# Performance work log

Measured on AMD Instinct MI355X. Metric: run time of the kernel, lower is better.

## Reference

```python
import jax, jax.numpy as jnp
import numpy as np

SF = 2  # shrink_factor


def resize_bilinear_ac(x, oh, ow):
    """Bilinear resize with align_corners=True, NCHW, matches torch F.interpolate."""
    B, C, H, W = x.shape
    if (oh, ow) == (H, W):
        return x
    ys = jnp.linspace(0.0, H - 1, oh)
    y0 = jnp.floor(ys).astype(jnp.int32)
    y1 = jnp.clip(y0 + 1, 0, H - 1)
    wy = (ys - y0).astype(x.dtype)
    xs = jnp.linspace(0.0, W - 1, ow)
    x0 = jnp.floor(xs).astype(jnp.int32)
    x1 = jnp.clip(x0 + 1, 0, W - 1)
    wx = (xs - x0).astype(x.dtype)
    t = x[:, :, y0, :] * (1 - wy)[None, None, :, None] + x[:, :, y1, :] * wy[None, None, :, None]
    return t[:, :, :, x0] * (1 - wx) + t[:, :, :, x1] * wx


def conv1x1(x, W, b):
    # x: [B,C,H,W], W: [O,C], b: [O]
    return jnp.einsum('bchw,oc->bohw', x, W) + b[None, :, None, None]


def setup_inputs() -> dict:
    key = jax.random.key(0)
    ks = jax.random.split(key, 8)
    B, C, H, W = 4, 512, 129, 129
    Cqk = C // 8
    s = 1.0 / np.sqrt(C)
    return {
        'x': jax.random.normal(ks[0], (B, C, H, W), jnp.float32),
        'Wq': jax.random.normal(ks[1], (Cqk, C), jnp.float32) * s,
        'bq': jax.random.normal(ks[2], (Cqk,), jnp.float32) * s,
        'Wk': jax.random.normal(ks[3], (Cqk, C), jnp.float32) * s,
        'bk': jax.random.normal(ks[4], (Cqk,), jnp.float32) * s,
        'Wv': jax.random.normal(ks[5], (C, C), jnp.float32) * s,
        'bv': jax.random.normal(ks[6], (C,), jnp.float32) * s,
        'gamma': jax.random.normal(ks[7], (1,), jnp.float32) * 0.1,
    }


def reference(x, Wq, bq, Wk, bk, Wv, bv, gamma):
    B, C, H, W = x.shape
    h = (H - 1) // SF + 1
    w = (W - 1) // SF + 1
    xs = resize_bilinear_ac(x, h, w)  # [B,C,h,w]
    N = h * w
    q = conv1x1(xs, Wq, bq).reshape(B, -1, N)  # [B,Cqk,N]
    k = conv1x1(xs, Wk, bk).reshape(B, -1, N)  # [B,Cqk,N]
    v = conv1x1(xs, Wv, bv).reshape(B, -1, N)  # [B,C,N]
    # energy[b,n,m] = <q[:,n], k[:,m]>
    energy = jnp.einsum('bcn,bcm->bnm', q, k)  # [B,N,N]
    attention = jax.nn.softmax(energy, axis=-1)
    # out[b,c,n] = sum_m v[b,c,m] * attention[b,n,m]  (bmm(value, attention^T))
    out = jnp.einsum('bcm,bnm->bcn', v, attention).reshape(B, C, h, w)
    Hu = (h - 1) * SF + 1
    Wu = (w - 1) * SF + 1
    out = resize_bilinear_ac(out, Hu, Wu)
    out = gamma[0] * out + x
    return out, energy
```

## Files before the change

kernel.cpp:

```cpp
#include <hip/hip_runtime.h>
#include <hip/hip_bf16.h>
#include <cstdint>

#define BB 4
#define CC 512
#define CQK 64
#define HH 129
#define WW 129
#define HS 65
#define WSZ 65
#define NN 4225
#define NP 4352
#define KPV 4288
#define OUTSZ 34080768
#define ESZ 17850625

typedef unsigned short u16;
typedef __attribute__((ext_vector_type(8))) __bf16 bfrag;
typedef __attribute__((ext_vector_type(4))) float f4v;

__device__ inline u16 f2bf(float f) {
    union { float f; unsigned int u; } v; v.f = f;
    unsigned int u = v.u;
    return (u16)((u + 0x7FFFu + ((u >> 16) & 1u)) >> 16);
}

__device__ __forceinline__ void gload16(const u16* g, u16* l) {
    __builtin_amdgcn_global_load_lds(
        (const __attribute__((address_space(1))) void*)g,
        (__attribute__((address_space(3))) void*)l, 16, 0, 0);
}

__global__ __launch_bounds__(256) void cast_weights(const float* __restrict__ Wq,
                                                    const float* __restrict__ Wk,
                                                    const float* __restrict__ Wv,
                                                    u16* __restrict__ Wc) {
    int idx = blockIdx.x * 256 + threadIdx.x;
    if (idx >= 640 * 512) return;
    int o = idx >> 9, c = idx & 511;
    float v = (o < 64) ? Wq[o * 512 + c] : (o < 128) ? Wk[(o - 64) * 512 + c] : Wv[(o - 128) * 512 + c];
    Wc[idx] = f2bf(v);
}

__global__ __launch_bounds__(256) void subsample_t(const float* __restrict__ x, u16* __restrict__ XsT) {
    __shared__ u16 tile[64][65];
    int nt = blockIdx.x, ct = blockIdx.y, b = blockIdx.z;
    int t = threadIdx.x;
#pragma unroll
    for (int l = 0; l < 16; ++l) {
        int e = t + l * 256;
        int ci = e >> 6, nj = e & 63;
        int n = nt * 64 + nj;
        int nc = n < (NN - 1) ? n : (NN - 1);
        int i = nc / 65, j = nc % 65;
        int c = ct * 64 + ci;
        float v = x[(((size_t)b * CC + c) * HH + 2 * i) * WW + 2 * j];
        tile[ci][nj] = f2bf(v);
    }
    __syncthreads();
#pragma unroll
    for (int l = 0; l < 16; ++l) {
        int e = t + l * 256;
        int nj = e >> 6, ci = e & 63;
        XsT[((size_t)b * NP + nt * 64 + nj) * 512 + ct * 64 + ci] = tile[ci][nj];
    }
}

template <int MODE>
__global__ __launch_bounds__(256) void gemm_nt(const u16* __restrict__ Abase,
                                               const u16* __restrict__ Bbase,
                                               int K, int lda, int ldb,
                                               float* __restrict__ outF,
                                               u16* __restrict__ out1, u16* __restrict__ out2,
                                               const float* __restrict__ bq,
                                               const float* __restrict__ bk,
                                               const float* __restrict__ bv,
                                               float* __restrict__ psums) {
    __shared__ __align__(16) u16 As[128 * 64];
    __shared__ __align__(16) u16 Bs[128 * 64];

    const int z = blockIdx.z;
    const u16* A; const u16* Bm;
    if (MODE == 0) { A = Abase;                          Bm = Bbase + (size_t)z * NP * 512; }
    if (MODE == 1) { A = Abase + (size_t)z * NP * 128;   Bm = Bbase + (size_t)z * NP * 128 + 64; }

    const size_t m0 = (size_t)blockIdx.y * 128;
    const size_t n0 = (size_t)blockIdx.x * 128;
    const u16* Ab = A + m0 * lda;
    const u16* Bb = Bm + n0 * ldb;

    const int tid = threadIdx.x;
    const int lane = tid & 63, w = tid >> 6;
    const int wr = w >> 1, wc = w & 1;
    const int frow = lane & 15, fk = (lane >> 4) * 8;

    f4v acc[4][4];
#pragma unroll
    for (int i = 0; i < 4; ++i)
#pragma unroll
        for (int j = 0; j < 4; ++j) acc[i][j] = (f4v){0.f, 0.f, 0.f, 0.f};

    for (int kt = 0; kt < K; kt += 64) {
        if (kt) __syncthreads();
#pragma unroll
        for (int it = 0; it < 4; ++it) {
            int cb = (it * 4 + w) * 64;
            int chunk = cb + lane;
            int r = chunk >> 3;
            int kc = (chunk & 7) << 3;
            gload16(Ab + (size_t)r * lda + kt + kc, &As[cb * 8]);
            gload16(Bb + (size_t)r * ldb + kt + kc, &Bs[cb * 8]);
        }
        __syncthreads();
#pragma unroll
        for (int ks = 0; ks < 2; ++ks) {
            bfrag af[4], bf[4];
#pragma unroll
            for (int i = 0; i < 4; ++i)
                af[i] = *(const bfrag*)&As[(wr * 64 + i * 16 + frow) * 64 + ks * 32 + fk];
#pragma unroll
            for (int j = 0; j < 4; ++j)
                bf[j] = *(const bfrag*)&Bs[(wc * 64 + j * 16 + frow) * 64 + ks * 32 + fk];
#pragma unroll
            for (int i = 0; i < 4; ++i)
#pragma unroll
                for (int j = 0; j < 4; ++j)
                    acc[i][j] = __builtin_amdgcn_mfma_f32_16x16x32_bf16(af[i], bf[j], acc[i][j], 0, 0, 0);
        }
    }

    const int rbase = (lane >> 4) * 4, cbase = lane & 15;

    if (MODE == 0) {
        u16* out1b = out1 + (size_t)z * NP * 128;
        u16* out2b = out2 + (size_t)z * 512 * NP;
#pragma unroll
        for (int i = 0; i < 4; ++i)
#pragma unroll
            for (int j = 0; j < 4; ++j) {
                size_t row0 = m0 + wr * 64 + i * 16 + rbase;
                size_t col = n0 + wc * 64 + j * 16 + cbase;
#pragma unroll
                for (int r = 0; r < 4; ++r) {
                    int o = (int)(row0 + r);
                    float bias = (o < 64) ? bq[o] : (o < 128) ? bk[o - 64] : bv[o - 128];
                    u16 bb = f2bf(acc[i][j][r] + bias);
                    if (o < 128) out1b[col * 128 + o] = bb;
                    else out2b[(size_t)(o - 128) * NP + col] = bb;
                }
            }
    } else {
        float* eb = outF + (size_t)z * ESZ;
        u16* Pb = out1 + (size_t)z * NP * NP;
        float psl[4][4];
#pragma unroll
        for (int i = 0; i < 4; ++i)
#pragma unroll
            for (int r = 0; r < 4; ++r) psl[i][r] = 0.f;
#pragma unroll
        for (int i = 0; i < 4; ++i)
#pragma unroll
            for (int j = 0; j < 4; ++j) {
                size_t row0 = m0 + wr * 64 + i * 16 + rbase;
                size_t col = n0 + wc * 64 + j * 16 + cbase;
#pragma unroll
                for (int r = 0; r < 4; ++r) {
                    float v = acc[i][j][r];
                    size_t ro = row0 + r;
                    float pe = (col < NN) ? __expf(v) : 0.f;
                    if (ro < NN && col < NN) eb[ro * NN + col] = v;
                    Pb[ro * NP + col] = f2bf(pe);
                    psl[i][r] += pe;
                }
            }
        float* pbase = psums + ((size_t)z * 68 + blockIdx.x * 2 + wc) * NP;
#pragma unroll
        for (int i = 0; i < 4; ++i)
#pragma unroll
            for (int r = 0; r < 4; ++r) {
                float s = psl[i][r];
                s += __shfl_xor(s, 1);
                s += __shfl_xor(s, 2);
                s += __shfl_xor(s, 4);
                s += __shfl_xor(s, 8);
                if (cbase == 0)
                    pbase[m0 + wr * 64 + i * 16 + rbase + r] = s;
            }
    }
}

__global__ __launch_bounds__(256) void reduce_sums(const float* __restrict__ psums,
                                                   float* __restrict__ invsum) {
    int idx = blockIdx.x * 256 + threadIdx.x;
    if (idx >= BB * NP) return;
    int b = idx / NP, n = idx % NP;
    const float* p = psums + (size_t)b * 68 * NP + n;
    float s = 0.f;
#pragma unroll
    for (int ct = 0; ct < 68; ++ct) s += p[(size_t)ct * NP];
    invsum[idx] = 1.f / s;
}

__global__ __launch_bounds__(256) void gemm_pv(const u16* __restrict__ Vb,
                                               const u16* __restrict__ P,
                                               float* __restrict__ ctx0,
                                               float* __restrict__ ctx1,
                                               const float* __restrict__ invsum) {
    __shared__ __align__(16) u16 As[128 * 64];
    __shared__ __align__(16) u16 Bs[128 * 64];

    unsigned flat = blockIdx.x + 34u * (blockIdx.y + 4u * blockIdx.z);
    unsigned swz = (flat & 7u) * 136u + (flat >> 3);
    unsigned zs = swz / 136u;
    unsigned rem = swz - zs * 136u;
    unsigned ys = rem / 34u;
    unsigned xs = rem - ys * 34u;
    const int b = (int)(zs >> 1), half = (int)(zs & 1);

    const u16* A = Vb + (size_t)b * 512 * NP;
    const u16* Bm = P + (size_t)b * NP * NP;
    const size_t m0 = (size_t)ys * 128;
    const size_t n0 = (size_t)xs * 128;
    const u16* Ab = A + m0 * NP;
    const u16* Bb = Bm + n0 * NP;
    const int kbeg = half ? 2176 : 0;
    const int kend = half ? KPV : 2176;

    const int tid = threadIdx.x;
    const int lane = tid & 63, w = tid >> 6;
    const int wr = w >> 1, wc = w & 1;
    const int frow = lane & 15, fk = (lane >> 4) * 8;

    f4v acc[4][4];
#pragma unroll
    for (int i = 0; i < 4; ++i)
#pragma unroll
        for (int j = 0; j < 4; ++j) acc[i][j] = (f4v){0.f, 0.f, 0.f, 0.f};

    for (int kt = kbeg; kt < kend; kt += 64) {
        if (kt != kbeg) __syncthreads();
#pragma unroll
        for (int it = 0; it < 4; ++it) {
            int cb = (it * 4 + w) * 64;
            int chunk = cb + lane;
            int r = chunk >> 3;
            int kc = (chunk & 7) << 3;
            gload16(Ab + (size_t)r * NP + kt + kc, &As[cb * 8]);
            gload16(Bb + (size_t)r * NP + kt + kc, &Bs[cb * 8]);
        }
        __syncthreads();
#pragma unroll
        for (int ks = 0; ks < 2; ++ks) {
            bfrag af[4], bf[4];
#pragma unroll
            for (int i = 0; i < 4; ++i)
                af[i] = *(const bfrag*)&As[(wr * 64 + i * 16 + frow) * 64 + ks * 32 + fk];
#pragma unroll
            for (int j = 0; j < 4; ++j)
                bf[j] = *(const bfrag*)&Bs[(wc * 64 + j * 16 + frow) * 64 + ks * 32 + fk];
#pragma unroll
            for (int i = 0; i < 4; ++i)
#pragma unroll
                for (int j = 0; j < 4; ++j)
                    acc[i][j] = __builtin_amdgcn_mfma_f32_16x16x32_bf16(af[i], bf[j], acc[i][j], 0, 0, 0);
        }
    }

    const int rbase = (lane >> 4) * 4, cbase = lane & 15;
    float* outFb = (half ? ctx1 : ctx0) + (size_t)b * 512 * NP;
    const float* isb = invsum + (size_t)b * NP;
#pragma unroll
    for (int j = 0; j < 4; ++j) {
        size_t col = n0 + wc * 64 + j * 16 + cbase;
        float inv = isb[col];
#pragma unroll
        for (int i = 0; i < 4; ++i) {
            size_t row0 = m0 + wr * 64 + i * 16 + rbase;
#pragma unroll
            for (int r = 0; r < 4; ++r)
                outFb[(row0 + r) * NP + col] = acc[i][j][r] * inv;
        }
    }
}

__global__ __launch_bounds__(256) void upsample_add(const float* __restrict__ ctx0,
                                                    const float* __restrict__ ctx1,
                                                    const float* __restrict__ x,
                                                    const float* __restrict__ gm,
                                                    float* __restrict__ out) {
    unsigned q = blockIdx.x * 256 + threadIdx.x;
    if (q >= (OUTSZ / 4)) return;
    unsigned idx0 = q * 4;
    float g = gm[0];
    float4 xv = *(const float4*)&x[idx0];
    float ov[4];
#pragma unroll
    for (int e = 0; e < 4; ++e) {
        unsigned idx = idx0 + e;
        unsigned xx = idx % WW;
        unsigned t = idx / WW;
        unsigned yy = t % HH;
        unsigned bc = t / HH;
        const float* cA = ctx0 + (size_t)bc * NP;
        const float* cB = ctx1 + (size_t)bc * NP;
        unsigned i0 = yy >> 1, j0 = xx >> 1;
        unsigned n00 = i0 * 65 + j0;
        float wy = 0.5f * (float)(yy & 1), wx = 0.5f * (float)(xx & 1);
        float c00 = cA[n00] + cB[n00];
        float c01 = cA[n00 + 1] + cB[n00 + 1];
        float c10 = cA[n00 + 65] + cB[n00 + 65];
        float c11 = cA[n00 + 66] + cB[n00 + 66];
        float cx0 = c00 + wx * (c01 - c00);
        float cx1 = c10 + wx * (c11 - c10);
        ov[e] = g * (cx0 + wy * (cx1 - cx0));
    }
    float4 o4 = {ov[0] + xv.x, ov[1] + xv.y, ov[2] + xv.z, ov[3] + xv.w};
    *(float4*)&out[idx0] = o4;
}

#define SZ_WC   ((size_t)640 * 512 * 2)
#define OFF_XST (SZ_WC)
#define SZ_XST  ((size_t)BB * NP * 512 * 2)
#define OFF_QKT (OFF_XST + SZ_XST)
#define SZ_QKT  ((size_t)BB * NP * 128 * 2)
#define OFF_V   (OFF_QKT + SZ_QKT)
#define SZ_V    ((size_t)BB * 512 * NP * 2)
#define OFF_CTX (OFF_V + SZ_V)
#define SZ_CTX  ((size_t)BB * 512 * NP * 4)
#define OFF_P   (OFF_CTX + SZ_CTX)
#define SZ_P    ((size_t)BB * NP * NP * 2)
#define OFF_INV (OFF_P + SZ_P)
#define SZ_INV  ((size_t)BB * NP * 4)
#define OFF_CTX2 (OFF_INV + SZ_INV)

extern "C" void kernel_launch(void* const* d_in, const int* in_sizes, int n_in,
                              void* d_out, int out_size, void* d_ws, size_t ws_size,
                              hipStream_t stream) {
    const float* x  = (const float*)d_in[0];
    const float* Wq = (const float*)d_in[1];
    const float* bq = (const float*)d_in[2];
    const float* Wk = (const float*)d_in[3];
    const float* bk = (const float*)d_in[4];
    const float* Wv = (const float*)d_in[5];
    const float* bv = (const float*)d_in[6];
    const float* gm = (const float*)d_in[7];

    float* out = (float*)d_out;
    float* energy = out + (size_t)OUTSZ;

    char* ws = (char*)d_ws;
    u16* Wc  = (u16*)(ws);
    u16* XsT = (u16*)(ws + OFF_XST);
    u16* qkT = (u16*)(ws + OFF_QKT);
    u16* V   = (u16*)(ws + OFF_V);
    float* ctx0 = (float*)(ws + OFF_CTX);
    float* psums = ctx0;
    u16* P   = (u16*)(ws + OFF_P);
    float* invsum = (float*)(ws + OFF_INV);
    float* ctx1 = (float*)(ws + OFF_CTX2);

    cast_weights<<<1280, 256, 0, stream>>>(Wq, Wk, Wv, Wc);
    subsample_t<<<dim3(68, 8, BB), 256, 0, stream>>>(x, XsT);
    gemm_nt<0><<<dim3(34, 5, BB), 256, 0, stream>>>(Wc, XsT, 512, 512, 512,
                                                    nullptr, qkT, V, bq, bk, bv, nullptr);
    gemm_nt<1><<<dim3(34, 34, BB), 256, 0, stream>>>(qkT, qkT, 64, 128, 128,
                                                     energy, P, nullptr, nullptr, nullptr, nullptr,
                                                     psums);
    reduce_sums<<<68, 256, 0, stream>>>(psums, invsum);
    gemm_pv<<<dim3(34, 4, 8), 256, 0, stream>>>(V, P, ctx0, ctx1, invsum);
    upsample_add<<<(OUTSZ / 4 + 255) / 256, 256, 0, stream>>>(ctx0, ctx1, x, gm, out);
}
```

Before: 475.1 us.

## Rewrite PV GEMM as 256x256 tiled, 4-way split-K, double-buffered swizzled-LDS kernel

Replaces the 128x128 PV GEMM with a 512-thread kernel using 256x256 output tiles, a 4-way K split and double-buffered, XOR-swizzled LDS. Global-to-LDS loads for the next k-slice are interleaved with MFMA phases, with explicit waitcnt, barriers and setprio. Partial context results are stored as bf16 in four slices, and the upsample kernel sums them. The aim is more data reuse per tile, overlap of loads with compute, and less partial-output traffic. The cost is an extra bf16 rounding of the partials and more slices for upsample to read.

```diff
diff --git a/kernel.cpp b/kernel.cpp
--- a/kernel.cpp
+++ b/kernel.cpp
@@ -11,9 +11,9 @@
 #define WSZ 65
 #define NN 4225
 #define NP 4352
-#define KPV 4288
 #define OUTSZ 34080768
 #define ESZ 17850625
+#define PVNT 17
 
 typedef unsigned short u16;
 typedef __attribute__((ext_vector_type(8))) __bf16 bfrag;
@@ -23,6 +23,9 @@
     union { float f; unsigned int u; } v; v.f = f;
     unsigned int u = v.u;
     return (u16)((u + 0x7FFFu + ((u >> 16) & 1u)) >> 16);
+}
+__device__ inline float bf2f(u16 v) {
+    union { unsigned u; float f; } x; x.u = (unsigned)v << 16; return x.f;
 }
 
 __device__ __forceinline__ void gload16(const u16* g, u16* l) {
@@ -201,90 +204,143 @@
     invsum[idx] = 1.f / s;
 }
 
-__global__ __launch_bounds__(256) void gemm_pv(const u16* __restrict__ Vb,
-                                               const u16* __restrict__ P,
-                                               float* __restrict__ ctx0,
-                                               float* __restrict__ ctx1,
-                                               const float* __restrict__ invsum) {
-    __shared__ __align__(16) u16 As[128 * 64];
-    __shared__ __align__(16) u16 Bs[128 * 64];
-
-    unsigned flat = blockIdx.x + 34u * (blockIdx.y + 4u * blockIdx.z);
-    unsigned swz = (flat & 7u) * 136u + (flat >> 3);
-    unsigned zs = swz / 136u;
-    unsigned rem = swz - zs * 136u;
-    unsigned ys = rem / 34u;
-    unsigned xs = rem - ys * 34u;
-    const int b = (int)(zs >> 1), half = (int)(zs & 1);
-
-    const u16* A = Vb + (size_t)b * 512 * NP;
-    const u16* Bm = P + (size_t)b * NP * NP;
-    const size_t m0 = (size_t)ys * 128;
-    const size_t n0 = (size_t)xs * 128;
-    const u16* Ab = A + m0 * NP;
-    const u16* Bb = Bm + n0 * NP;
-    const int kbeg = half ? 2176 : 0;
-    const int kend = half ? KPV : 2176;
+__global__ __launch_bounds__(512, 2) void gemm_pv8(const u16* __restrict__ Vb,
+                                                   const u16* __restrict__ P,
+                                                   u16* __restrict__ ctxp,
+                                                   const float* __restrict__ invsum) {
+    __shared__ u16 lds[65536];
+
+    unsigned flat = blockIdx.x;
+    unsigned wg = (flat & 7u) * 68u + (flat >> 3);
+    unsigned ntile = wg / 32u;
+    unsigned r = wg - ntile * 32u;
+    unsigned mt = r >> 4;
+    unsigned b = (r >> 2) & 3u;
+    unsigned s = r & 3u;
+    const unsigned c0 = mt * 256u, n0 = ntile * 256u;
+    const unsigned kbeg = s * (PVNT * 64u);
+
+    const u16* Apan = Vb + (size_t)b * 512 * NP + (size_t)c0 * NP;
+    const u16* Bpan = P + (size_t)b * NP * NP + (size_t)n0 * NP;
 
     const int tid = threadIdx.x;
     const int lane = tid & 63, w = tid >> 6;
-    const int wr = w >> 1, wc = w & 1;
-    const int frow = lane & 15, fk = (lane >> 4) * 8;
-
-    f4v acc[4][4];
-#pragma unroll
-    for (int i = 0; i < 4; ++i)
+    const int wr = w >> 2, wc = w & 3;
+
+    auto stage = [&](int buf, int op, int kh, int tile) {
+        const u16* gp = op ? Bpan : Apan;
+        unsigned kg = kbeg + (unsigned)tile * 64u + (unsigned)kh * 32u;
+        int ubase = ((buf * 2 + op) * 2 + kh) * 8192;
+#pragma unroll
+        for (int l = 0; l < 2; ++l) {
+            int X = (w * 2 + l) * 1024 + lane * 16;
+            int S = X ^ ((X >> 3) & 0x30);
+            int row = S >> 6, kb = S & 63;
+            const u16* g = gp + (size_t)row * NP + kg + (kb >> 1);
+            gload16(g, &lds[ubase + (w * 2 + l) * 512]);
+        }
+    };
+    auto rdfrag = [&](int buf, int op, int rowbase, int ks) -> bfrag {
+        int row = rowbase + (lane & 15);
+        int d = row * 64 + (lane >> 4) * 16;
+        d ^= (d >> 3) & 0x30;
+        int ubase = ((buf * 2 + op) * 2 + ks) * 8192;
+        return *(const bfrag*)((const char*)lds + (size_t)ubase * 2 + d);
+    };
+
+    f4v acc[8][4];
+#pragma unroll
+    for (int i = 0; i < 8; ++i)
 #pragma unroll
         for (int j = 0; j < 4; ++j) acc[i][j] = (f4v){0.f, 0.f, 0.f, 0.f};
 
-    for (int kt = kbeg; kt < kend; kt += 64) {
-        if (kt != kbeg) __syncthreads();
-#pragma unroll
-        for (int it = 0; it < 4; ++it) {
-            int cb = (it * 4 + w) * 64;
-            int chunk = cb + lane;
-            int r = chunk >> 3;
-            int kc = (chunk & 7) << 3;
-            gload16(Ab + (size_t)r * NP + kt + kc, &As[cb * 8]);
-            gload16(Bb + (size_t)r * NP + kt + kc, &Bs[cb * 8]);
+    stage(0, 0, 0, 0); stage(0, 1, 0, 0);
+    stage(0, 0, 1, 0); stage(0, 1, 1, 0);
+    stage(1, 0, 0, 1); stage(1, 1, 0, 1);
+    asm volatile("s_waitcnt vmcnt(8)" ::: "memory");
+    asm volatile("s_barrier" ::: "memory");
+
+    int buf = 0;
+#pragma unroll 1
+    for (int t = 0; t < PVNT; ++t) {
+        const int nb = buf ^ 1;
+        bfrag a0, a1, a2, a3, b0, b1, b2, b3;
+        b0 = rdfrag(buf, 1, wc * 64 + 0, 0);  b1 = rdfrag(buf, 1, wc * 64 + 16, 0);
+        b2 = rdfrag(buf, 1, wc * 64 + 32, 0); b3 = rdfrag(buf, 1, wc * 64 + 48, 0);
+        a0 = rdfrag(buf, 0, wr * 128 + 0, 0);  a1 = rdfrag(buf, 0, wr * 128 + 16, 0);
+        a2 = rdfrag(buf, 0, wr * 128 + 32, 0); a3 = rdfrag(buf, 0, wr * 128 + 48, 0);
+        if (t + 1 < PVNT) stage(nb, 0, 1, t + 1);
+        asm volatile("s_barrier" ::: "memory");
+        __builtin_amdgcn_s_setprio(1);
+#define MF(i, A, B, j) acc[i][j] = __builtin_amdgcn_mfma_f32_16x16x32_bf16(A, B, acc[i][j], 0, 0, 0)
+        MF(0, a0, b0, 0); MF(0, a0, b1, 1); MF(0, a0, b2, 2); MF(0, a0, b3, 3);
+        MF(1, a1, b0, 0); MF(1, a1, b1, 1); MF(1, a1, b2, 2); MF(1, a1, b3, 3);
+        MF(2, a2, b0, 0); MF(2, a2, b1, 1); MF(2, a2, b2, 2); MF(2, a2, b3, 3);
+        MF(3, a3, b0, 0); MF(3, a3, b1, 1); MF(3, a3, b2, 2); MF(3, a3, b3, 3);
+        __builtin_amdgcn_s_setprio(0);
+        asm volatile("s_barrier" ::: "memory");
+        a0 = rdfrag(buf, 0, wr * 128 + 64, 0);  a1 = rdfrag(buf, 0, wr * 128 + 80, 0);
+        a2 = rdfrag(buf, 0, wr * 128 + 96, 0);  a3 = rdfrag(buf, 0, wr * 128 + 112, 0);
+        if (t + 1 < PVNT) stage(nb, 1, 1, t + 1);
+        if (t < PVNT - 1) asm volatile("s_waitcnt vmcnt(8)" ::: "memory");
+        else              asm volatile("s_waitcnt vmcnt(0)" ::: "memory");
+        asm volatile("s_barrier" ::: "memory");
+        __builtin_amdgcn_s_setprio(1);
+        MF(4, a0, b0, 0); MF(4, a0, b1, 1); MF(4, a0, b2, 2); MF(4, a0, b3, 3);
+        MF(5, a1, b0, 0); MF(5, a1, b1, 1); MF(5, a1, b2, 2); MF(5, a1, b3, 3);
+        MF(6, a2, b0, 0); MF(6, a2, b1, 1); MF(6, a2, b2, 2); MF(6, a2, b3, 3);
+        MF(7, a3, b0, 0); MF(7, a3, b1, 1); MF(7, a3, b2, 2); MF(7, a3, b3, 3);
+        __builtin_amdgcn_s_setprio(0);
+        asm volatile("s_barrier" ::: "memory");
+        b0 = rdfrag(buf, 1, wc * 64 + 0, 1);  b1 = rdfrag(buf, 1, wc * 64 + 16, 1);
+        b2 = rdfrag(buf, 1, wc * 64 + 32, 1); b3 = rdfrag(buf, 1, wc * 64 + 48, 1);
+        a0 = rdfrag(buf, 0, wr * 128 + 0, 1);  a1 = rdfrag(buf, 0, wr * 128 + 16, 1);
+        a2 = rdfrag(buf, 0, wr * 128 + 32, 1); a3 = rdfrag(buf, 0, wr * 128 + 48, 1);
+        if (t + 2 < PVNT) stage(buf, 0, 0, t + 2);
+        asm volatile("s_barrier" ::: "memory");
+        __builtin_amdgcn_s_setprio(1);
+        MF(0, a0, b0, 0); MF(0, a0, b1, 1); MF(0, a0, b2, 2); MF(0, a0, b3, 3);
+        MF(1, a1, b0, 0); MF(1, a1, b1, 1); MF(1, a1, b2, 2); MF(1, a1, b3, 3);
+        MF(2, a2, b0, 0); MF(2, a2, b1, 1); MF(2, a2, b2, 2); MF(2, a2, b3, 3);
+        MF(3, a3, b0, 0); MF(3, a3, b1, 1); MF(3, a3, b2, 2); MF(3, a3, b3, 3);
+        __builtin_amdgcn_s_setprio(0);
+        asm volatile("s_barrier" ::: "memory");
+        a0 = rdfrag(buf, 0, wr * 128 + 64, 1);  a1 = rdfrag(buf, 0, wr * 128 + 80, 1);
+        a2 = rdfrag(buf, 0, wr * 128 + 96, 1);  a3 = rdfrag(buf, 0, wr * 128 + 112, 1);
+        if (t + 2 < PVNT) stage(buf, 1, 0, t + 2);
+        if (t < PVNT - 2)       asm volatile("s_waitcnt vmcnt(8)" ::: "memory");
+        else if (t == PVNT - 2) asm volatile("s_waitcnt vmcnt(4)" ::: "memory");
+        asm volatile("s_barrier" ::: "memory");
+        __builtin_amdgcn_s_setprio(1);
+        MF(4, a0, b0, 0); MF(4, a0, b1, 1); MF(4, a0, b2, 2); MF(4, a0, b3, 3);
+        MF(5, a1, b0, 0); MF(5, a1, b1, 1); MF(5, a1, b2, 2); MF(5, a1, b3, 3);
+        MF(6, a2, b0, 0); MF(6, a2, b1, 1); MF(6, a2, b2, 2); MF(6, a2, b3, 3);
+        MF(7, a3, b0, 0); MF(7, a3, b1, 1); MF(7, a3, b2, 2); MF(7, a3, b3, 3);
+        __builtin_amdgcn_s_setprio(0);
+        asm volatile("s_barrier" ::: "memory");
+#undef MF
+        buf = nb;
+    }
+
+    const int rbase = (lane >> 4) * 4, cbase = lane & 15;
+    u16* cb = ctxp + ((size_t)(s * BB + b) * 512 + c0) * NP;
+    const float* isb = invsum + (size_t)b * NP;
+#pragma unroll
+    for (int j = 0; j < 4; ++j) {
+        unsigned n = n0 + wc * 64 + j * 16 + cbase;
+        float inv = isb[n];
+#pragma unroll
+        for (int i = 0; i < 8; ++i) {
+            unsigned row = wr * 128 + i * 16 + rbase;
+#pragma unroll
+            for (int rr = 0; rr < 4; ++rr)
+                cb[(size_t)(row + rr) * NP + n] = f2bf(acc[i][j][rr] * inv);
         }
-        __syncthreads();
-#pragma unroll
-        for (int ks = 0; ks < 2; ++ks) {
-            bfrag af[4], bf[4];
-#pragma unroll
-            for (int i = 0; i < 4; ++i)
-                af[i] = *(const bfrag*)&As[(wr * 64 + i * 16 + frow) * 64 + ks * 32 + fk];
-#pragma unroll
-            for (int j = 0; j < 4; ++j)
-                bf[j] = *(const bfrag*)&Bs[(wc * 64 + j * 16 + frow) * 64 + ks * 32 + fk];
-#pragma unroll
-            for (int i = 0; i < 4; ++i)
-#pragma unroll
-                for (int j = 0; j < 4; ++j)
-                    acc[i][j] = __builtin_amdgcn_mfma_f32_16x16x32_bf16(af[i], bf[j], acc[i][j], 0, 0, 0);
-        }
-    }
-
-    const int rbase = (lane >> 4) * 4, cbase = lane & 15;
-    float* outFb = (half ? ctx1 : ctx0) + (size_t)b * 512 * NP;
-    const float* isb = invsum + (size_t)b * NP;
-#pragma unroll
-    for (int j = 0; j < 4; ++j) {
-        size_t col = n0 + wc * 64 + j * 16 + cbase;
-        float inv = isb[col];
-#pragma unroll
-        for (int i = 0; i < 4; ++i) {
-            size_t row0 = m0 + wr * 64 + i * 16 + rbase;
-#pragma unroll
-            for (int r = 0; r < 4; ++r)
-                outFb[(row0 + r) * NP + col] = acc[i][j][r] * inv;
-        }
-    }
-}
-
-__global__ __launch_bounds__(256) void upsample_add(const float* __restrict__ ctx0,
-                                                    const float* __restrict__ ctx1,
+    }
+}
+
+#define SLICE ((size_t)BB * 512 * NP)
+__global__ __launch_bounds__(256) void upsample_add(const u16* __restrict__ ctxp,
                                                     const float* __restrict__ x,
                                                     const float* __restrict__ gm,
                                                     float* __restrict__ out) {
@@ -301,15 +357,19 @@
         unsigned t = idx / WW;
         unsigned yy = t % HH;
         unsigned bc = t / HH;
-        const float* cA = ctx0 + (size_t)bc * NP;
-        const float* cB = ctx1 + (size_t)bc * NP;
+        const u16* cb = ctxp + (size_t)bc * NP;
         unsigned i0 = yy >> 1, j0 = xx >> 1;
         unsigned n00 = i0 * 65 + j0;
         float wy = 0.5f * (float)(yy & 1), wx = 0.5f * (float)(xx & 1);
-        float c00 = cA[n00] + cB[n00];
-        float c01 = cA[n00 + 1] + cB[n00 + 1];
-        float c10 = cA[n00 + 65] + cB[n00 + 65];
-        float c11 = cA[n00 + 66] + cB[n00 + 66];
+        float c00 = 0.f, c01 = 0.f, c10 = 0.f, c11 = 0.f;
+#pragma unroll
+        for (int sl = 0; sl < 4; ++sl) {
+            const u16* p = cb + (size_t)sl * SLICE;
+            c00 += bf2f(p[n00]);
+            c01 += bf2f(p[n00 + 1]);
+            c10 += bf2f(p[n00 + 65]);
+            c11 += bf2f(p[n00 + 66]);
+        }
         float cx0 = c00 + wx * (c01 - c00);
         float cx1 = c10 + wx * (c11 - c10);
         ov[e] = g * (cx0 + wy * (cx1 - cx0));
@@ -318,20 +378,20 @@
     *(float4*)&out[idx0] = o4;
 }
 
-#define SZ_WC   ((size_t)640 * 512 * 2)
-#define OFF_XST (SZ_WC)
-#define SZ_XST  ((size_t)BB * NP * 512 * 2)
-#define OFF_QKT (OFF_XST + SZ_XST)
-#define SZ_QKT  ((size_t)BB * NP * 128 * 2)
-#define OFF_V   (OFF_QKT + SZ_QKT)
-#define SZ_V    ((size_t)BB * 512 * NP * 2)
-#define OFF_CTX (OFF_V + SZ_V)
-#define SZ_CTX  ((size_t)BB * 512 * NP * 4)
-#define OFF_P   (OFF_CTX + SZ_CTX)
-#define SZ_P    ((size_t)BB * NP * NP * 2)
-#define OFF_INV (OFF_P + SZ_P)
-#define SZ_INV  ((size_t)BB * NP * 4)
-#define OFF_CTX2 (OFF_INV + SZ_INV)
+#define SZ_WC    ((size_t)640 * 512 * 2)
+#define OFF_XST  (SZ_WC)
+#define SZ_XST   ((size_t)BB * NP * 512 * 2)
+#define OFF_QKT  (OFF_XST + SZ_XST)
+#define SZ_QKT   ((size_t)BB * NP * 128 * 2)
+#define OFF_V    (OFF_QKT + SZ_QKT)
+#define SZ_V     ((size_t)BB * 512 * NP * 2)
+#define OFF_PS   (OFF_V + SZ_V)
+#define SZ_PS    ((size_t)BB * 68 * NP * 4)
+#define OFF_INV  (OFF_PS + SZ_PS)
+#define SZ_INV   ((size_t)BB * NP * 4)
+#define OFF_CTXP (OFF_INV + SZ_INV)
+#define SZ_CTXP  ((size_t)4 * BB * 512 * NP * 2)
+#define OFF_P    (OFF_CTXP + SZ_CTXP)
 
 extern "C" void kernel_launch(void* const* d_in, const int* in_sizes, int n_in,
                               void* d_out, int out_size, void* d_ws, size_t ws_size,
@@ -349,15 +409,14 @@
     float* energy = out + (size_t)OUTSZ;
 
     char* ws = (char*)d_ws;
-    u16* Wc  = (u16*)(ws);
-    u16* XsT = (u16*)(ws + OFF_XST);
-    u16* qkT = (u16*)(ws + OFF_QKT);
-    u16* V   = (u16*)(ws + OFF_V);
-    float* ctx0 = (float*)(ws + OFF_CTX);
-    float* psums = ctx0;
-    u16* P   = (u16*)(ws + OFF_P);
+    u16* Wc    = (u16*)(ws);
+    u16* XsT   = (u16*)(ws + OFF_XST);
+    u16* qkT   = (u16*)(ws + OFF_QKT);
+    u16* V     = (u16*)(ws + OFF_V);
+    float* psums  = (float*)(ws + OFF_PS);
     float* invsum = (float*)(ws + OFF_INV);
-    float* ctx1 = (float*)(ws + OFF_CTX2);
+    u16* ctxp  = (u16*)(ws + OFF_CTXP);
+    u16* P     = (u16*)(ws + OFF_P);
 
     cast_weights<<<1280, 256, 0, stream>>>(Wq, Wk, Wv, Wc);
     subsample_t<<<dim3(68, 8, BB), 256, 0, stream>>>(x, XsT);
@@ -367,6 +426,6 @@
                                                      energy, P, nullptr, nullptr, nullptr, nullptr,
                                                      psums);
     reduce_sums<<<68, 256, 0, stream>>>(psums, invsum);
-    gemm_pv<<<dim3(34, 4, 8), 256, 0, stream>>>(V, P, ctx0, ctx1, invsum);
-    upsample_add<<<(OUTSZ / 4 + 255) / 256, 256, 0, stream>>>(ctx0, ctx1, x, gm, out);
-}
+    gemm_pv8<<<544, 512, 0, stream>>>(V, P, ctxp, invsum);
+    upsample_add<<<(OUTSZ / 4 + 255) / 256, 256, 0, stream>>>(ctxp, x, gm, out);
+}
```

New measurement: 495.3 us. 1.04x slower.

## Stage GEMM epilogues through LDS for coalesced stores, store context as bf16

Applied to the files above, without the earlier changes.

The P tile in the QK^T GEMM and the context tile in the PV GEMM are now written to shared memory first, then copied out to global memory as contiguous 16-byte row stores instead of scattered 2-byte or 4-byte stores. The two split-K context partials are stored as bf16 rather than fp32, which halves their traffic in both the writing GEMM and the upsample kernel. The PV block swizzle is also reordered so consecutive blocks share a P column tile. The cost is two extra barriers and an LDS round trip per tile, plus lower precision in the context partials.

```diff
diff --git a/kernel.cpp b/kernel.cpp
--- a/kernel.cpp
+++ b/kernel.cpp
@@ -24,6 +24,9 @@
     unsigned int u = v.u;
     return (u16)((u + 0x7FFFu + ((u >> 16) & 1u)) >> 16);
 }
+__device__ inline float bf2f(u16 v) {
+    union { unsigned u; float f; } x; x.u = (unsigned)v << 16; return x.f;
+}
 
 __device__ __forceinline__ void gload16(const u16* g, u16* l) {
     __builtin_amdgcn_global_load_lds(
@@ -76,8 +79,9 @@
                                                const float* __restrict__ bk,
                                                const float* __restrict__ bv,
                                                float* __restrict__ psums) {
-    __shared__ __align__(16) u16 As[128 * 64];
-    __shared__ __align__(16) u16 Bs[128 * 64];
+    __shared__ __align__(16) u16 S[16384];
+    u16* As = S;
+    u16* Bs = S + 8192;
 
     const int z = blockIdx.z;
     const u16* A; const u16* Bm;
@@ -157,19 +161,23 @@
         for (int i = 0; i < 4; ++i)
 #pragma unroll
             for (int r = 0; r < 4; ++r) psl[i][r] = 0.f;
+
+        __syncthreads();
 #pragma unroll
         for (int i = 0; i < 4; ++i)
 #pragma unroll
             for (int j = 0; j < 4; ++j) {
-                size_t row0 = m0 + wr * 64 + i * 16 + rbase;
-                size_t col = n0 + wc * 64 + j * 16 + cbase;
+                int rl = wr * 64 + i * 16 + rbase;
+                int cl = wc * 64 + j * 16 + cbase;
+                size_t row0 = m0 + rl;
+                size_t col = n0 + cl;
 #pragma unroll
                 for (int r = 0; r < 4; ++r) {
                     float v = acc[i][j][r];
                     size_t ro = row0 + r;
                     float pe = (col < NN) ? __expf(v) : 0.f;
                     if (ro < NN && col < NN) eb[ro * NN + col] = v;
-                    Pb[ro * NP + col] = f2bf(pe);
+                    S[(rl + r) * 128 + cl] = f2bf(pe);
                     psl[i][r] += pe;
                 }
             }
@@ -186,6 +194,14 @@
                 if (cbase == 0)
                     pbase[m0 + wr * 64 + i * 16 + rbase + r] = s;
             }
+        __syncthreads();
+        u16* pb = Pb + m0 * NP + n0;
+#pragma unroll
+        for (int l = 0; l < 8; ++l) {
+            int idx = tid + l * 256;
+            int row = idx >> 4, c16 = idx & 15;
+            *(int4*)(pb + (size_t)row * NP + c16 * 8) = *(const int4*)&S[row * 128 + c16 * 8];
+        }
     }
 }
 
@@ -203,18 +219,18 @@
 
 __global__ __launch_bounds__(256) void gemm_pv(const u16* __restrict__ Vb,
                                                const u16* __restrict__ P,
-                                               float* __restrict__ ctx0,
-                                               float* __restrict__ ctx1,
+                                               u16* __restrict__ ctxp,
                                                const float* __restrict__ invsum) {
-    __shared__ __align__(16) u16 As[128 * 64];
-    __shared__ __align__(16) u16 Bs[128 * 64];
+    __shared__ __align__(16) u16 S[16384];
+    u16* As = S;
+    u16* Bs = S + 8192;
 
     unsigned flat = blockIdx.x + 34u * (blockIdx.y + 4u * blockIdx.z);
     unsigned swz = (flat & 7u) * 136u + (flat >> 3);
     unsigned zs = swz / 136u;
     unsigned rem = swz - zs * 136u;
-    unsigned ys = rem / 34u;
-    unsigned xs = rem - ys * 34u;
+    unsigned xs = rem >> 2;
+    unsigned ys = rem & 3u;
     const int b = (int)(zs >> 1), half = (int)(zs & 1);
 
     const u16* A = Vb + (size_t)b * 512 * NP;
@@ -267,24 +283,32 @@
     }
 
     const int rbase = (lane >> 4) * 4, cbase = lane & 15;
-    float* outFb = (half ? ctx1 : ctx0) + (size_t)b * 512 * NP;
     const float* isb = invsum + (size_t)b * NP;
+    __syncthreads();
 #pragma unroll
     for (int j = 0; j < 4; ++j) {
-        size_t col = n0 + wc * 64 + j * 16 + cbase;
-        float inv = isb[col];
+        int cl = wc * 64 + j * 16 + cbase;
+        float inv = isb[n0 + cl];
 #pragma unroll
         for (int i = 0; i < 4; ++i) {
-            size_t row0 = m0 + wr * 64 + i * 16 + rbase;
+            int rl = wr * 64 + i * 16 + rbase;
 #pragma unroll
             for (int r = 0; r < 4; ++r)
-                outFb[(row0 + r) * NP + col] = acc[i][j][r] * inv;
-        }
-    }
-}
-
-__global__ __launch_bounds__(256) void upsample_add(const float* __restrict__ ctx0,
-                                                    const float* __restrict__ ctx1,
+                S[(rl + r) * 128 + cl] = f2bf(acc[i][j][r] * inv);
+        }
+    }
+    __syncthreads();
+    u16* cb = ctxp + ((size_t)(half * BB + b) * 512 + m0) * NP + n0;
+#pragma unroll
+    for (int l = 0; l < 8; ++l) {
+        int idx = tid + l * 256;
+        int row = idx >> 4, c16 = idx & 15;
+        *(int4*)(cb + (size_t)row * NP + c16 * 8) = *(const int4*)&S[row * 128 + c16 * 8];
+    }
+}
+
+#define SLICE ((size_t)BB * 512 * NP)
+__global__ __launch_bounds__(256) void upsample_add(const u16* __restrict__ ctxp,
                                                     const float* __restrict__ x,
                                                     const float* __restrict__ gm,
                                                     float* __restrict__ out) {
@@ -301,15 +325,19 @@
         unsigned t = idx / WW;
         unsigned yy = t % HH;
         unsigned bc = t / HH;
-        const float* cA = ctx0 + (size_t)bc * NP;
-        const float* cB = ctx1 + (size_t)bc * NP;
+        const u16* cb = ctxp + (size_t)bc * NP;
         unsigned i0 = yy >> 1, j0 = xx >> 1;
         unsigned n00 = i0 * 65 + j0;
         float wy = 0.5f * (float)(yy & 1), wx = 0.5f * (float)(xx & 1);
-        float c00 = cA[n00] + cB[n00];
-        float c01 = cA[n00 + 1] + cB[n00 + 1];
-        float c10 = cA[n00 + 65] + cB[n00 + 65];
-        float c11 = cA[n00 + 66] + cB[n00 + 66];
+        float c00 = 0.f, c01 = 0.f, c10 = 0.f, c11 = 0.f;
+#pragma unroll
+        for (int sl = 0; sl < 2; ++sl) {
+            const u16* p = cb + (size_t)sl * SLICE;
+            c00 += bf2f(p[n00]);
+            c01 += bf2f(p[n00 + 1]);
+            c10 += bf2f(p[n00 + 65]);
+            c11 += bf2f(p[n00 + 66]);
+        }
         float cx0 = c00 + wx * (c01 - c00);
         float cx1 = c10 + wx * (c11 - c10);
         ov[e] = g * (cx0 + wy * (cx1 - cx0));
@@ -318,20 +346,20 @@
     *(float4*)&out[idx0] = o4;
 }
 
-#define SZ_WC   ((size_t)640 * 512 * 2)
-#define OFF_XST (SZ_WC)
-#define SZ_XST  ((size_t)BB * NP * 512 * 2)
-#define OFF_QKT (OFF_XST + SZ_XST)
-#define SZ_QKT  ((size_t)BB * NP * 128 * 2)
-#define OFF_V   (OFF_QKT + SZ_QKT)
-#define SZ_V    ((size_t)BB * 512 * NP * 2)
-#define OFF_CTX (OFF_V + SZ_V)
-#define SZ_CTX  ((size_t)BB * 512 * NP * 4)
-#define OFF_P   (OFF_CTX + SZ_CTX)
-#define SZ_P    ((size_t)BB * NP * NP * 2)
-#define OFF_INV (OFF_P + SZ_P)
-#define SZ_INV  ((size_t)BB * NP * 4)
-#define OFF_CTX2 (OFF_INV + SZ_INV)
+#define SZ_WC    ((size_t)640 * 512 * 2)
+#define OFF_XST  (SZ_WC)
+#define SZ_XST   ((size_t)BB * NP * 512 * 2)
+#define OFF_QKT  (OFF_XST + SZ_XST)
+#define SZ_QKT   ((size_t)BB * NP * 128 * 2)
+#define OFF_V    (OFF_QKT + SZ_QKT)
+#define SZ_V     ((size_t)BB * 512 * NP * 2)
+#define OFF_PS   (OFF_V + SZ_V)
+#define SZ_PS    ((size_t)BB * 68 * NP * 4)
+#define OFF_INV  (OFF_PS + SZ_PS)
+#define SZ_INV   ((size_t)BB * NP * 4)
+#define OFF_CTXP (OFF_INV + SZ_INV)
+#define SZ_CTXP  ((size_t)2 * BB * 512 * NP * 2)
+#define OFF_P    (OFF_CTXP + SZ_CTXP)
 
 extern "C" void kernel_launch(void* const* d_in, const int* in_sizes, int n_in,
                               void* d_out, int out_size, void* d_ws, size_t ws_size,
@@ -349,15 +377,14 @@
     float* energy = out + (size_t)OUTSZ;
 
     char* ws = (char*)d_ws;
-    u16* Wc  = (u16*)(ws);
-    u16* XsT = (u16*)(ws + OFF_XST);
-    u16* qkT = (u16*)(ws + OFF_QKT);
-    u16* V   = (u16*)(ws + OFF_V);
-    float* ctx0 = (float*)(ws + OFF_CTX);
-    float* psums = ctx0;
-    u16* P   = (u16*)(ws + OFF_P);
+    u16* Wc    = (u16*)(ws);
+    u16* XsT   = (u16*)(ws + OFF_XST);
+    u16* qkT   = (u16*)(ws + OFF_QKT);
+    u16* V     = (u16*)(ws + OFF_V);
+    float* psums  = (float*)(ws + OFF_PS);
     float* invsum = (float*)(ws + OFF_INV);
-    float* ctx1 = (float*)(ws + OFF_CTX2);
+    u16* ctxp  = (u16*)(ws + OFF_CTXP);
+    u16* P     = (u16*)(ws + OFF_P);
 
     cast_weights<<<1280, 256, 0, stream>>>(Wq, Wk, Wv, Wc);
     subsample_t<<<dim3(68, 8, BB), 256, 0, stream>>>(x, XsT);
@@ -367,6 +394,6 @@
                                                      energy, P, nullptr, nullptr, nullptr, nullptr,
                                                      psums);
     reduce_sums<<<68, 256, 0, stream>>>(psums, invsum);
-    gemm_pv<<<dim3(34, 4, 8), 256, 0, stream>>>(V, P, ctx0, ctx1, invsum);
-    upsample_add<<<(OUTSZ / 4 + 255) / 256, 256, 0, stream>>>(ctx0, ctx1, x, gm, out);
-}
+    gemm_pv<<<dim3(34, 4, 8), 256, 0, stream>>>(V, P, ctxp, invsum);
+    upsample_add<<<(OUTSZ / 4 + 255) / 256, 256, 0, stream>>>(ctxp, x, gm, out);
+}
```

Result: faster. 460.8 us (-3.0%).
